# Performance work log

Hardware: AMD Instinct MI355X
Metric: run time of the kernel (lower is better)

Reference implementation:

```python
import jax, jax.numpy as jnp
import numpy as np

B, LQ, LP, H = 16, 2048, 2048, 1024

def setup_inputs() -> dict:
    key = jax.random.key(0)
    kq, kp, kw = jax.random.split(key, 3)
    q = jax.random.normal(kq, (B, LQ, H), dtype=jnp.float32)
    p = jax.random.normal(kp, (B, LP, H), dtype=jnp.float32)
    W = jax.random.normal(kw, (H, H), dtype=jnp.float32) * (1.0 / np.sqrt(H))
    b = jnp.zeros((H,), dtype=jnp.float32)
    return {"q": q, "p": p, "W": W, "b": b}

def reference(q, p, W, b):
    # shared linear + ReLU projections (torch Linear: x @ W.T + b)
    q_lin = jax.nn.relu(jnp.einsum('bqh,oh->bqo', q, W) + b)  # [B,LQ,H]
    p_lin = jax.nn.relu(jnp.einsum('bph,oh->bpo', p, W) + b)  # [B,LP,H]
    # unscaled cross-attention scores: p_lin @ q_lin^T -> [B,LP,LQ]
    scores = jnp.einsum('bpd,bqd->bpq', p_lin, q_lin)
    att = jax.nn.softmax(scores, axis=2)
    # context-aware query: att @ q_lin -> [B,LP,H]
    return jnp.einsum('bpq,bqd->bpd', att, q_lin)
```

## Files before the change

### kernel.cpp

```cpp
#include <hip/hip_runtime.h>


#define LQN 2048
#define LPN 2048
#define HD  1024
#define NBATCH 16

typedef _Float16 half8 __attribute__((ext_vector_type(8)));
typedef _Float16 half4_t __attribute__((ext_vector_type(4)));
typedef float f32x4 __attribute__((ext_vector_type(4)));

#define GLP(src, dst) __builtin_amdgcn_global_load_lds(                          \
    (const __attribute__((address_space(1))) void*)(src),                        \
    (__attribute__((address_space(3))) void*)(dst), 16, 0, 0)

__global__ __launch_bounds__(256) void cvt_f32_f16(const float* __restrict__ in,
                                                   _Float16* __restrict__ out,
                                                   long n4) {
  long i0 = (long)blockIdx.x * blockDim.x + threadIdx.x;
  long stride = (long)gridDim.x * blockDim.x;
  for (long i = i0; i < n4; i += stride) {
    float4 v = ((const float4*)in)[i];
    half4_t h = {(_Float16)v.x, (_Float16)v.y, (_Float16)v.z, (_Float16)v.w};
    ((half4_t*)out)[i] = h;
  }
}

__global__ __launch_bounds__(256) void transpose_k(const _Float16* __restrict__ in,
                                                   _Float16* __restrict__ out) {
  __shared__ _Float16 t[64][72];
  const int bz = blockIdx.z;
  const int q0 = blockIdx.x * 64;
  const int d0 = blockIdx.y * 64;
  const int tt = threadIdx.x;
  const int ql = tt & 63, dg = tt >> 6;
  const _Float16* src = in + ((size_t)bz * LQN + q0 + ql) * HD + d0 + dg * 16;
  half8 v0 = *(const half8*)(src);
  half8 v1 = *(const half8*)(src + 8);
  int g0 = (dg * 2) ^ (ql & 7);
  int g1 = (dg * 2 + 1) ^ (ql & 7);
  *(half8*)&t[ql][g0 * 8] = v0;
  *(half8*)&t[ql][g1 * 8] = v1;
  __syncthreads();
  const int dl = tt & 63, qg = tt >> 6;
  half8 o0, o1;
#pragma unroll
  for (int j = 0; j < 8; ++j) {
    int qq = qg * 16 + j;
    o0[j] = t[qq][(((dl >> 3) ^ (qq & 7)) << 3) + (dl & 7)];
  }
#pragma unroll
  for (int j = 0; j < 8; ++j) {
    int qq = qg * 16 + 8 + j;
    o1[j] = t[qq][(((dl >> 3) ^ (qq & 7)) << 3) + (dl & 7)];
  }
  _Float16* dst = out + ((size_t)bz * HD + d0 + dl) * LQN + q0 + qg * 16;
  *(half8*)dst = o0;
  *(half8*)(dst + 8) = o1;
}


#define SYNC_PRE                                        \
  __builtin_amdgcn_s_barrier();                         \
  __builtin_amdgcn_s_setprio(1);

#define SYNC_POST                                       \
  __builtin_amdgcn_s_setprio(0);                        \
  __builtin_amdgcn_s_barrier();                         \
  __builtin_amdgcn_sched_barrier(0);

#define SYNC_POST_VM                                    \
  __builtin_amdgcn_s_setprio(0);                        \
  asm volatile("s_waitcnt vmcnt(4)" ::: "memory");      \
  __builtin_amdgcn_s_barrier();                         \
  __builtin_amdgcn_sched_barrier(0);

#define LOADA(qm, buf)                                                            \
  _Pragma("unroll")                                                               \
  for (int mi = 0; mi < 4; ++mi) {                                                \
    areg[mi][0] = *(const half8*)(smA + (buf)*32768 + a0 + ((qm)*4+mi)*4096);     \
    areg[mi][1] = *(const half8*)(smA + (buf)*32768 + a1 + ((qm)*4+mi)*4096);     \
  }

#define LOADB(qn, buf)                                                            \
  _Pragma("unroll")                                                               \
  for (int ni = 0; ni < 2; ++ni) {                                                \
    bregs[qn][ni][0] = *(const half8*)(smB + (buf)*32768 + b0 + ((qn)*2+ni)*8192);\
    bregs[qn][ni][1] = *(const half8*)(smB + (buf)*32768 + b1 + ((qn)*2+ni)*8192);\
  }

#define STAGEA(t, h, buf) do {                                                    \
  GLP(gA + (size_t)((h)*128)*lda + (size_t)(t)*64,                                \
      smW + (buf)*32768 + (h)*16384 + wid*1024);                                  \
  GLP(gA + (size_t)((h)*128+64)*lda + (size_t)(t)*64,                             \
      smW + (buf)*32768 + (h)*16384 + 8192 + wid*1024);                           \
} while (0)

#define STAGEB(t, h, buf) do {                                                    \
  GLP(gB + (size_t)((h)*128)*ldb + (size_t)(t)*64,                                \
      smW + 65536 + (buf)*32768 + (h)*16384 + wid*1024);                          \
  GLP(gB + (size_t)((h)*128+64)*ldb + (size_t)(t)*64,                             \
      smW + 65536 + (buf)*32768 + (h)*16384 + 8192 + wid*1024);                   \
} while (0)

#define DO_MFMA(qm, qn)                                                           \
  _Pragma("unroll")                                                               \
  for (int mi = 0; mi < 4; ++mi) {                                                \
    _Pragma("unroll")                                                             \
    for (int ni = 0; ni < 2; ++ni) {                                              \
      acc[(qm)*4+mi][(qn)*2+ni] = __builtin_amdgcn_mfma_f32_16x16x32_f16(         \
          areg[mi][0], bregs[qn][ni][0], acc[(qm)*4+mi][(qn)*2+ni], 0, 0, 0);     \
      acc[(qm)*4+mi][(qn)*2+ni] = __builtin_amdgcn_mfma_f32_16x16x32_f16(         \
          areg[mi][1], bregs[qn][ni][1], acc[(qm)*4+mi][(qn)*2+ni], 0, 0, 0);     \
    }                                                                             \
  }

template <int EPI>
__global__ __launch_bounds__(512, 2) void gemm8p(
    const _Float16* __restrict__ A, const _Float16* __restrict__ B,
    const float* __restrict__ bias, void* __restrict__ Cv,
    float2* __restrict__ side, int K, int lda, int ldb, int ldc,
    long sAz, long sBz, long sCz) {
  extern __shared__ __align__(16) char smem[];
  const char* smA = smem;
  const char* smB = smem + 65536;
  char* smW = smem;

  const int tid = threadIdx.x;
  const int lane = tid & 63, wid = tid >> 6;
  const int l16 = lane & 15, lhi = lane >> 4;
  const int wr = wid >> 2, wcn = wid & 3;

  const int nx = gridDim.x;
  const int d = blockIdx.y * nx + blockIdx.x;
  const int cpx = (nx * gridDim.y) >> 3;
  const int t_ = (d & 7) * cpx + (d >> 3);
  const int xsh = 31 - __builtin_clz(nx);
  const int bn0 = (t_ & (nx - 1)) << 8;
  const int bm0 = (t_ >> xsh) << 8;

  const int mask = (l16 & 7) << 4;
  const int a0 = (wr * 2048 + l16 * 128 + lhi * 16) ^ mask;
  const int a1 = a0 ^ 64;
  const int b0 = (wcn * 2048 + l16 * 128 + lhi * 16) ^ mask;
  const int b1 = b0 ^ 64;

  const int srow = tid >> 3;
  const int scol = (((tid & 7) ^ ((tid >> 3) & 7)) << 3);

  const _Float16* gA = A + (size_t)blockIdx.z * sAz + (size_t)(bm0 + srow) * lda + scol;
  const _Float16* gB = B + (size_t)blockIdx.z * sBz + (size_t)(bn0 + srow) * ldb + scol;

  const int NT = K >> 6, NI = K >> 7;

  f32x4 acc[8][4] = {};
  half8 areg[4][2], bregs[2][2][2];

  STAGEA(0, 0, 0); STAGEB(0, 0, 0);
  STAGEA(0, 1, 0); STAGEB(0, 1, 0);
  STAGEA(1, 0, 1); STAGEB(1, 0, 1);
  __builtin_amdgcn_sched_barrier(0);
  asm volatile("s_waitcnt vmcnt(4)" ::: "memory");
  __builtin_amdgcn_s_barrier();
  __builtin_amdgcn_sched_barrier(0);

  for (int i = 0; i < NI; ++i) {
    const int t1 = 2 * i + 1;
    int t2 = 2 * i + 2; if (t2 > NT - 1) t2 = NT - 1;
    int t3 = 2 * i + 3; if (t3 > NT - 1) t3 = NT - 1;
    STAGEA(t1, 1, 1); LOADA(0, 0) LOADB(0, 0)
    SYNC_PRE DO_MFMA(0, 0) SYNC_POST
    STAGEB(t1, 1, 1); LOADB(1, 0)
    SYNC_PRE DO_MFMA(0, 1) SYNC_POST
    STAGEA(t2, 0, 0); LOADA(1, 0)
    SYNC_PRE DO_MFMA(1, 0) SYNC_POST
    STAGEB(t2, 0, 0);
    SYNC_PRE DO_MFMA(1, 1) SYNC_POST_VM
    STAGEA(t2, 1, 0); LOADA(0, 1) LOADB(0, 1)
    SYNC_PRE DO_MFMA(0, 0) SYNC_POST
    STAGEB(t2, 1, 0); LOADB(1, 1)
    SYNC_PRE DO_MFMA(0, 1) SYNC_POST
    STAGEA(t3, 0, 1); LOADA(1, 1)
    SYNC_PRE DO_MFMA(1, 0) SYNC_POST
    STAGEB(t3, 0, 1);
    SYNC_PRE DO_MFMA(1, 1) SYNC_POST_VM
  }

  if constexpr (EPI == 0) {
    float* Cb = (float*)Cv + (size_t)blockIdx.z * sCz;
#pragma unroll
    for (int m = 0; m < 8; ++m) {
      int row0 = bm0 + m * 32 + wr * 16 + lhi * 4;
#pragma unroll
      for (int n = 0; n < 4; ++n) {
        int col = bn0 + n * 64 + wcn * 16 + l16;
#pragma unroll
        for (int v = 0; v < 4; ++v)
          Cb[(size_t)(row0 + v) * ldc + col] = acc[m][n][v];
      }
    }
  } else if constexpr (EPI == 1) {
    _Float16* Cb = (_Float16*)Cv;
#pragma unroll
    for (int n = 0; n < 4; ++n) {
      int col = bn0 + n * 64 + wcn * 16 + l16;
      float bv = bias[col];
#pragma unroll
      for (int m = 0; m < 8; ++m) {
        int row0 = bm0 + m * 32 + wr * 16 + lhi * 4;
        Cb[(size_t)(row0 + 0) * ldc + col] = (_Float16)fmaxf(acc[m][n][0] + bv, 0.f);
        Cb[(size_t)(row0 + 1) * ldc + col] = (_Float16)fmaxf(acc[m][n][1] + bv, 0.f);
        Cb[(size_t)(row0 + 2) * ldc + col] = (_Float16)fmaxf(acc[m][n][2] + bv, 0.f);
        Cb[(size_t)(row0 + 3) * ldc + col] = (_Float16)fmaxf(acc[m][n][3] + bv, 0.f);
      }
    }
  } else {
    float* redm = (float*)smW;
    float* reds = (float*)(smW + 4096);
    float tm[8][4];
#pragma unroll
    for (int m = 0; m < 8; ++m)
#pragma unroll
      for (int v = 0; v < 4; ++v)
        tm[m][v] = fmaxf(fmaxf(acc[m][0][v], acc[m][1][v]),
                         fmaxf(acc[m][2][v], acc[m][3][v]));
#pragma unroll
    for (int o = 1; o < 16; o <<= 1)
#pragma unroll
      for (int m = 0; m < 8; ++m)
#pragma unroll
        for (int v = 0; v < 4; ++v)
          tm[m][v] = fmaxf(tm[m][v], __shfl_xor(tm[m][v], o));
    __syncthreads();
    if (l16 == 0) {
#pragma unroll
      for (int m = 0; m < 8; ++m)
#pragma unroll
        for (int v = 0; v < 4; ++v)
          redm[(m * 32 + wr * 16 + lhi * 4 + v) * 4 + wcn] = tm[m][v];
    }
    __syncthreads();
    float rm[8][4], rs[8][4];
#pragma unroll
    for (int m = 0; m < 8; ++m)
#pragma unroll
      for (int v = 0; v < 4; ++v) {
        float4 q4 = ((const float4*)redm)[m * 32 + wr * 16 + lhi * 4 + v];
        rm[m][v] = fmaxf(fmaxf(q4.x, q4.y), fmaxf(q4.z, q4.w));
      }
#pragma unroll
    for (int m = 0; m < 8; ++m)
#pragma unroll
      for (int v = 0; v < 4; ++v) {
        float s = 0.f;
#pragma unroll
        for (int n = 0; n < 4; ++n) {
          float e = __expf(acc[m][n][v] - rm[m][v]);
          acc[m][n][v] = e;
          s += e;
        }
        tm[m][v] = s;
      }
#pragma unroll
    for (int o = 1; o < 16; o <<= 1)
#pragma unroll
      for (int m = 0; m < 8; ++m)
#pragma unroll
        for (int v = 0; v < 4; ++v)
          tm[m][v] += __shfl_xor(tm[m][v], o);
    __syncthreads();
    if (l16 == 0) {
#pragma unroll
      for (int m = 0; m < 8; ++m)
#pragma unroll
        for (int v = 0; v < 4; ++v)
          reds[(m * 32 + wr * 16 + lhi * 4 + v) * 4 + wcn] = tm[m][v];
    }
    __syncthreads();
#pragma unroll
    for (int m = 0; m < 8; ++m)
#pragma unroll
      for (int v = 0; v < 4; ++v) {
        float4 q4 = ((const float4*)reds)[m * 32 + wr * 16 + lhi * 4 + v];
        rs[m][v] = (q4.x + q4.y) + (q4.z + q4.w);
      }
    _Float16* Cb = (_Float16*)Cv + (size_t)blockIdx.z * sCz;
#pragma unroll
    for (int n = 0; n < 4; ++n) {
      int col = bn0 + n * 64 + wcn * 16 + l16;
#pragma unroll
      for (int m = 0; m < 8; ++m) {
        int row0 = bm0 + m * 32 + wr * 16 + lhi * 4;
        Cb[(size_t)(row0 + 0) * ldc + col] = (_Float16)acc[m][n][0];
        Cb[(size_t)(row0 + 1) * ldc + col] = (_Float16)acc[m][n][1];
        Cb[(size_t)(row0 + 2) * ldc + col] = (_Float16)acc[m][n][2];
        Cb[(size_t)(row0 + 3) * ldc + col] = (_Float16)acc[m][n][3];
      }
    }
    if (l16 == 0 && wcn == 0) {
      float2* sb = side + ((size_t)blockIdx.z * 2048 + bm0) * 8 + (bn0 >> 8);
#pragma unroll
      for (int m = 0; m < 8; ++m)
#pragma unroll
        for (int v = 0; v < 4; ++v) {
          int r = m * 32 + wr * 16 + lhi * 4 + v;
          sb[(size_t)r * 8] = make_float2(rm[m][v], rs[m][v]);
        }
    }
  }
}

__global__ __launch_bounds__(256) void renorm_k(_Float16* __restrict__ P,
                                                const float2* __restrict__ side) {
  const int row = blockIdx.x;
  const int bz = blockIdx.y;
  const float2* sd = side + ((size_t)bz * 2048 + row) * 8;
  float mt[8], st[8];
#pragma unroll
  for (int t = 0; t < 8; ++t) { float2 v = sd[t]; mt[t] = v.x; st[t] = v.y; }
  float m = mt[0];
#pragma unroll
  for (int t = 1; t < 8; ++t) m = fmaxf(m, mt[t]);
  float S = 0.f;
#pragma unroll
  for (int t = 0; t < 8; ++t) S += st[t] * __expf(mt[t] - m);
  const float inv = 1.f / S;
  const int tid = threadIdx.x;
  const float sc = __expf(mt[tid >> 5] - m) * inv;
  _Float16* p = P + (((size_t)bz * 2048 + row) * 2048) + tid * 8;
  half8 v = *(half8*)p;
#pragma unroll
  for (int j = 0; j < 8; ++j) v[j] = (_Float16)((float)v[j] * sc);
  *(half8*)p = v;
}

extern "C" void kernel_launch(void* const* d_in, const int* in_sizes, int n_in,
                              void* d_out, int out_size, void* d_ws, size_t ws_size,
                              hipStream_t stream) {
  const float* q = (const float*)d_in[0];
  const float* p = (const float*)d_in[1];
  const float* W = (const float*)d_in[2];
  const float* bias = (const float*)d_in[3];
  float* out = (float*)d_out;
  char* ws = (char*)d_ws;

  _Float16* qf    = (_Float16*)(ws);
  _Float16* pf    = (_Float16*)(ws + 67108864L);
  _Float16* qlin  = (_Float16*)(ws + 134217728L);
  _Float16* plin  = (_Float16*)(ws + 201326592L);
  _Float16* qlinT = (_Float16*)(ws + 268435456L);
  _Float16* Wf    = (_Float16*)(ws + 335544320L);
  _Float16* Pbuf  = (_Float16*)(ws);
  float2*   side  = (float2*)(ws + 67108864L);

  const long nQ = (long)NBATCH * LQN * HD;
  const size_t SH = 131072;

  cvt_f32_f16<<<2048, 256, 0, stream>>>(q, qf, nQ / 4);
  cvt_f32_f16<<<2048, 256, 0, stream>>>(p, pf, nQ / 4);
  cvt_f32_f16<<<64, 256, 0, stream>>>(W, Wf, (long)HD * HD / 4);

  gemm8p<1><<<dim3(HD / 256, 2 * NBATCH * LQN / 256, 1), 512, SH, stream>>>(
      qf, Wf, bias, qlin, (float2*)0, HD, HD, HD, HD, 0, 0, 0);

  transpose_k<<<dim3(LQN / 64, HD / 64, NBATCH), 256, 0, stream>>>(qlin, qlinT);

  for (int c = 0; c < 2; ++c) {
    int bz0 = c * 8;
    gemm8p<2><<<dim3(LQN / 256, LPN / 256, 8), 512, SH, stream>>>(
        plin + (size_t)bz0 * LPN * HD, qlin + (size_t)bz0 * LQN * HD,
        (const float*)0, Pbuf, side,
        HD, HD, HD, LQN,
        (long)LPN * HD, (long)LQN * HD, (long)LPN * LQN);
    renorm_k<<<dim3(LPN, 8), 256, 0, stream>>>(Pbuf, side);
    gemm8p<0><<<dim3(HD / 256, LPN / 256, 8), 512, SH, stream>>>(
        Pbuf, qlinT + (size_t)bz0 * HD * LQN,
        (const float*)0, out + (size_t)bz0 * LPN * HD, (float2*)0,
        LQN, LQN, LQN, HD,
        (long)LPN * LQN, (long)HD * LQN, (long)LPN * HD);
  }
}
```

Measured before the change: 591.1 us.

## Fuse qlin transpose into projection epilogue and double-buffer GEMM fragment registers

The separate transpose kernel is removed. The projection GEMM epilogue now also writes qlin transposed as half4 stores for the q rows. The GEMM main loop is reorganised to use two sets of A/B register fragments, so LDS reads for the next sub-tile are issued one MFMA phase ahead of their use, with the staging order and vmcnt waits reshuffled to match. The aim is to save one kernel launch plus a full read and write of qlin, and to hide LDS latency behind MFMAs. The costs are higher register pressure and scattered strided transposed stores in the epilogue.

```diff
diff --git a/kernel.cpp b/kernel.cpp
--- a/kernel.cpp
+++ b/kernel.cpp
@@ -26,41 +26,9 @@
   }
 }
 
-__global__ __launch_bounds__(256) void transpose_k(const _Float16* __restrict__ in,
-                                                   _Float16* __restrict__ out) {
-  __shared__ _Float16 t[64][72];
-  const int bz = blockIdx.z;
-  const int q0 = blockIdx.x * 64;
-  const int d0 = blockIdx.y * 64;
-  const int tt = threadIdx.x;
-  const int ql = tt & 63, dg = tt >> 6;
-  const _Float16* src = in + ((size_t)bz * LQN + q0 + ql) * HD + d0 + dg * 16;
-  half8 v0 = *(const half8*)(src);
-  half8 v1 = *(const half8*)(src + 8);
-  int g0 = (dg * 2) ^ (ql & 7);
-  int g1 = (dg * 2 + 1) ^ (ql & 7);
-  *(half8*)&t[ql][g0 * 8] = v0;
-  *(half8*)&t[ql][g1 * 8] = v1;
-  __syncthreads();
-  const int dl = tt & 63, qg = tt >> 6;
-  half8 o0, o1;
-#pragma unroll
-  for (int j = 0; j < 8; ++j) {
-    int qq = qg * 16 + j;
-    o0[j] = t[qq][(((dl >> 3) ^ (qq & 7)) << 3) + (dl & 7)];
-  }
-#pragma unroll
-  for (int j = 0; j < 8; ++j) {
-    int qq = qg * 16 + 8 + j;
-    o1[j] = t[qq][(((dl >> 3) ^ (qq & 7)) << 3) + (dl & 7)];
-  }
-  _Float16* dst = out + ((size_t)bz * HD + d0 + dl) * LQN + q0 + qg * 16;
-  *(half8*)dst = o0;
-  *(half8*)(dst + 8) = o1;
-}
-
 
 #define SYNC_PRE                                        \
+  __builtin_amdgcn_sched_barrier(0);                    \
   __builtin_amdgcn_s_barrier();                         \
   __builtin_amdgcn_s_setprio(1);
 
@@ -75,18 +43,18 @@
   __builtin_amdgcn_s_barrier();                         \
   __builtin_amdgcn_sched_barrier(0);
 
-#define LOADA(qm, buf)                                                            \
+#define LOADA_TO(dst, qm, buf)                                                    \
   _Pragma("unroll")                                                               \
   for (int mi = 0; mi < 4; ++mi) {                                                \
-    areg[mi][0] = *(const half8*)(smA + (buf)*32768 + a0 + ((qm)*4+mi)*4096);     \
-    areg[mi][1] = *(const half8*)(smA + (buf)*32768 + a1 + ((qm)*4+mi)*4096);     \
-  }
-
-#define LOADB(qn, buf)                                                            \
+    dst[mi][0] = *(const half8*)(smA + (buf)*32768 + a0 + ((qm)*4+mi)*4096);      \
+    dst[mi][1] = *(const half8*)(smA + (buf)*32768 + a1 + ((qm)*4+mi)*4096);      \
+  }
+
+#define LOADB_TO(dst, qn, buf)                                                    \
   _Pragma("unroll")                                                               \
   for (int ni = 0; ni < 2; ++ni) {                                                \
-    bregs[qn][ni][0] = *(const half8*)(smB + (buf)*32768 + b0 + ((qn)*2+ni)*8192);\
-    bregs[qn][ni][1] = *(const half8*)(smB + (buf)*32768 + b1 + ((qn)*2+ni)*8192);\
+    dst[ni][0] = *(const half8*)(smB + (buf)*32768 + b0 + ((qn)*2+ni)*8192);      \
+    dst[ni][1] = *(const half8*)(smB + (buf)*32768 + b1 + ((qn)*2+ni)*8192);      \
   }
 
 #define STAGEA(t, h, buf) do {                                                    \
@@ -103,15 +71,15 @@
       smW + 65536 + (buf)*32768 + (h)*16384 + 8192 + wid*1024);                   \
 } while (0)
 
-#define DO_MFMA(qm, qn)                                                           \
+#define DO_MFMA2(aset, bset, qm, qn)                                              \
   _Pragma("unroll")                                                               \
   for (int mi = 0; mi < 4; ++mi) {                                                \
     _Pragma("unroll")                                                             \
     for (int ni = 0; ni < 2; ++ni) {                                              \
       acc[(qm)*4+mi][(qn)*2+ni] = __builtin_amdgcn_mfma_f32_16x16x32_f16(         \
-          areg[mi][0], bregs[qn][ni][0], acc[(qm)*4+mi][(qn)*2+ni], 0, 0, 0);     \
+          aset[mi][0], bset[ni][0], acc[(qm)*4+mi][(qn)*2+ni], 0, 0, 0);          \
       acc[(qm)*4+mi][(qn)*2+ni] = __builtin_amdgcn_mfma_f32_16x16x32_f16(         \
-          areg[mi][1], bregs[qn][ni][1], acc[(qm)*4+mi][(qn)*2+ni], 0, 0, 0);     \
+          aset[mi][1], bset[ni][1], acc[(qm)*4+mi][(qn)*2+ni], 0, 0, 0);          \
     }                                                                             \
   }
 
@@ -119,8 +87,8 @@
 __global__ __launch_bounds__(512, 2) void gemm8p(
     const _Float16* __restrict__ A, const _Float16* __restrict__ B,
     const float* __restrict__ bias, void* __restrict__ Cv,
-    float2* __restrict__ side, int K, int lda, int ldb, int ldc,
-    long sAz, long sBz, long sCz) {
+    _Float16* __restrict__ CT, float2* __restrict__ side,
+    int K, int lda, int ldb, int ldc, long sAz, long sBz, long sCz) {
   extern __shared__ __align__(16) char smem[];
   const char* smA = smem;
   const char* smB = smem + 65536;
@@ -154,36 +122,35 @@
   const int NT = K >> 6, NI = K >> 7;
 
   f32x4 acc[8][4] = {};
-  half8 areg[4][2], bregs[2][2][2];
-
-  STAGEA(0, 0, 0); STAGEB(0, 0, 0);
-  STAGEA(0, 1, 0); STAGEB(0, 1, 0);
-  STAGEA(1, 0, 1); STAGEB(1, 0, 1);
+  half8 aA0[4][2], aA1[4][2], bs0[2][2], bs1[2][2];
+
+  STAGEA(0, 0, 0); STAGEA(0, 1, 0); STAGEB(0, 0, 0); STAGEB(0, 1, 0);
+  STAGEA(1, 0, 1); STAGEA(1, 1, 1); STAGEB(1, 0, 1);
   __builtin_amdgcn_sched_barrier(0);
-  asm volatile("s_waitcnt vmcnt(4)" ::: "memory");
+  asm volatile("s_waitcnt vmcnt(6)" ::: "memory");
   __builtin_amdgcn_s_barrier();
   __builtin_amdgcn_sched_barrier(0);
+  LOADA_TO(aA0, 0, 0) LOADB_TO(bs0, 0, 0)
 
   for (int i = 0; i < NI; ++i) {
-    const int t1 = 2 * i + 1;
-    int t2 = 2 * i + 2; if (t2 > NT - 1) t2 = NT - 1;
-    int t3 = 2 * i + 3; if (t3 > NT - 1) t3 = NT - 1;
-    STAGEA(t1, 1, 1); LOADA(0, 0) LOADB(0, 0)
-    SYNC_PRE DO_MFMA(0, 0) SYNC_POST
-    STAGEB(t1, 1, 1); LOADB(1, 0)
-    SYNC_PRE DO_MFMA(0, 1) SYNC_POST
-    STAGEA(t2, 0, 0); LOADA(1, 0)
-    SYNC_PRE DO_MFMA(1, 0) SYNC_POST
-    STAGEB(t2, 0, 0);
-    SYNC_PRE DO_MFMA(1, 1) SYNC_POST_VM
-    STAGEA(t2, 1, 0); LOADA(0, 1) LOADB(0, 1)
-    SYNC_PRE DO_MFMA(0, 0) SYNC_POST
-    STAGEB(t2, 1, 0); LOADB(1, 1)
-    SYNC_PRE DO_MFMA(0, 1) SYNC_POST
-    STAGEA(t3, 0, 1); LOADA(1, 1)
-    SYNC_PRE DO_MFMA(1, 0) SYNC_POST
-    STAGEB(t3, 0, 1);
-    SYNC_PRE DO_MFMA(1, 1) SYNC_POST_VM
+    int t2c = 2 * i + 2; if (t2c > NT - 1) t2c = NT - 1;
+    int t3c = 2 * i + 3; if (t3c > NT - 1) t3c = NT - 1;
+    STAGEB(2 * i + 1, 1, 1); LOADB_TO(bs1, 1, 0) LOADA_TO(aA1, 1, 0)
+    SYNC_PRE DO_MFMA2(aA0, bs0, 0, 0) SYNC_POST
+    STAGEA(t2c, 0, 0);
+    SYNC_PRE DO_MFMA2(aA0, bs1, 0, 1) SYNC_POST
+    STAGEA(t2c, 1, 0);
+    SYNC_PRE DO_MFMA2(aA1, bs0, 1, 0) SYNC_POST_VM
+    STAGEB(t2c, 0, 0); LOADA_TO(aA0, 0, 1) LOADB_TO(bs0, 0, 1)
+    SYNC_PRE DO_MFMA2(aA1, bs1, 1, 1) SYNC_POST
+    STAGEB(t2c, 1, 0); LOADB_TO(bs1, 1, 1) LOADA_TO(aA1, 1, 1)
+    SYNC_PRE DO_MFMA2(aA0, bs0, 0, 0) SYNC_POST
+    STAGEA(t3c, 0, 1);
+    SYNC_PRE DO_MFMA2(aA0, bs1, 0, 1) SYNC_POST
+    STAGEA(t3c, 1, 1);
+    SYNC_PRE DO_MFMA2(aA1, bs0, 1, 0) SYNC_POST_VM
+    STAGEB(t3c, 0, 1); LOADA_TO(aA0, 0, 0) LOADB_TO(bs0, 0, 0)
+    SYNC_PRE DO_MFMA2(aA1, bs1, 1, 1) SYNC_POST
   }
 
   if constexpr (EPI == 0) {
@@ -201,6 +168,7 @@
     }
   } else if constexpr (EPI == 1) {
     _Float16* Cb = (_Float16*)Cv;
+    const bool doCT = (bm0 < NBATCH * LQN);
 #pragma unroll
     for (int n = 0; n < 4; ++n) {
       int col = bn0 + n * 64 + wcn * 16 + l16;
@@ -208,10 +176,19 @@
 #pragma unroll
       for (int m = 0; m < 8; ++m) {
         int row0 = bm0 + m * 32 + wr * 16 + lhi * 4;
-        Cb[(size_t)(row0 + 0) * ldc + col] = (_Float16)fmaxf(acc[m][n][0] + bv, 0.f);
-        Cb[(size_t)(row0 + 1) * ldc + col] = (_Float16)fmaxf(acc[m][n][1] + bv, 0.f);
-        Cb[(size_t)(row0 + 2) * ldc + col] = (_Float16)fmaxf(acc[m][n][2] + bv, 0.f);
-        Cb[(size_t)(row0 + 3) * ldc + col] = (_Float16)fmaxf(acc[m][n][3] + bv, 0.f);
+        float v0 = fmaxf(acc[m][n][0] + bv, 0.f);
+        float v1 = fmaxf(acc[m][n][1] + bv, 0.f);
+        float v2 = fmaxf(acc[m][n][2] + bv, 0.f);
+        float v3 = fmaxf(acc[m][n][3] + bv, 0.f);
+        Cb[(size_t)(row0 + 0) * ldc + col] = (_Float16)v0;
+        Cb[(size_t)(row0 + 1) * ldc + col] = (_Float16)v1;
+        Cb[(size_t)(row0 + 2) * ldc + col] = (_Float16)v2;
+        Cb[(size_t)(row0 + 3) * ldc + col] = (_Float16)v3;
+        if (doCT) {
+          half4_t h = {(_Float16)v0, (_Float16)v1, (_Float16)v2, (_Float16)v3};
+          int bz = row0 >> 11, qi = row0 & 2047;
+          *(half4_t*)&CT[(size_t)bz * ((size_t)HD * LQN) + (size_t)col * LQN + qi] = h;
+        }
       }
     }
   } else {
@@ -361,21 +338,19 @@
   cvt_f32_f16<<<64, 256, 0, stream>>>(W, Wf, (long)HD * HD / 4);
 
   gemm8p<1><<<dim3(HD / 256, 2 * NBATCH * LQN / 256, 1), 512, SH, stream>>>(
-      qf, Wf, bias, qlin, (float2*)0, HD, HD, HD, HD, 0, 0, 0);
-
-  transpose_k<<<dim3(LQN / 64, HD / 64, NBATCH), 256, 0, stream>>>(qlin, qlinT);
+      qf, Wf, bias, qlin, qlinT, (float2*)0, HD, HD, HD, HD, 0, 0, 0);
 
   for (int c = 0; c < 2; ++c) {
     int bz0 = c * 8;
     gemm8p<2><<<dim3(LQN / 256, LPN / 256, 8), 512, SH, stream>>>(
         plin + (size_t)bz0 * LPN * HD, qlin + (size_t)bz0 * LQN * HD,
-        (const float*)0, Pbuf, side,
+        (const float*)0, Pbuf, (_Float16*)0, side,
         HD, HD, HD, LQN,
         (long)LPN * HD, (long)LQN * HD, (long)LPN * LQN);
     renorm_k<<<dim3(LPN, 8), 256, 0, stream>>>(Pbuf, side);
     gemm8p<0><<<dim3(HD / 256, LPN / 256, 8), 512, SH, stream>>>(
         Pbuf, qlinT + (size_t)bz0 * HD * LQN,
-        (const float*)0, out + (size_t)bz0 * LPN * HD, (float2*)0,
+        (const float*)0, out + (size_t)bz0 * LPN * HD, (_Float16*)0, (float2*)0,
         LQN, LQN, LQN, HD,
         (long)LPN * LQN, (long)HD * LQN, (long)LPN * HD);
   }
```

Result: slower. 825.5 us (+39.7%).

## Merge GEMM pipeline phases to halve barriers per K-iteration

Applied to the files above, without the earlier changes.

Restructures the main GEMM loop from eight barrier-separated phases into four. Each phase now issues both A and B global-to-LDS stages, loads both B fragment sets, and runs two MFMA quadrants back to back. The aim is to cut the number of workgroup barriers and priority switches per iteration. In exchange, global-load issue and MFMA are interleaved less finely, and the vmcnt(4) wait now covers a different mix of loads.

```diff
diff --git a/kernel.cpp b/kernel.cpp
--- a/kernel.cpp
+++ b/kernel.cpp
@@ -75,18 +75,18 @@
   __builtin_amdgcn_s_barrier();                         \
   __builtin_amdgcn_sched_barrier(0);
 
-#define LOADA(qm, buf)                                                            \
+#define LOADA_TO(dst, qm, buf)                                                    \
   _Pragma("unroll")                                                               \
   for (int mi = 0; mi < 4; ++mi) {                                                \
-    areg[mi][0] = *(const half8*)(smA + (buf)*32768 + a0 + ((qm)*4+mi)*4096);     \
-    areg[mi][1] = *(const half8*)(smA + (buf)*32768 + a1 + ((qm)*4+mi)*4096);     \
-  }
-
-#define LOADB(qn, buf)                                                            \
+    dst[mi][0] = *(const half8*)(smA + (buf)*32768 + a0 + ((qm)*4+mi)*4096);      \
+    dst[mi][1] = *(const half8*)(smA + (buf)*32768 + a1 + ((qm)*4+mi)*4096);      \
+  }
+
+#define LOADB_TO(dst, qn, buf)                                                    \
   _Pragma("unroll")                                                               \
   for (int ni = 0; ni < 2; ++ni) {                                                \
-    bregs[qn][ni][0] = *(const half8*)(smB + (buf)*32768 + b0 + ((qn)*2+ni)*8192);\
-    bregs[qn][ni][1] = *(const half8*)(smB + (buf)*32768 + b1 + ((qn)*2+ni)*8192);\
+    dst[ni][0] = *(const half8*)(smB + (buf)*32768 + b0 + ((qn)*2+ni)*8192);      \
+    dst[ni][1] = *(const half8*)(smB + (buf)*32768 + b1 + ((qn)*2+ni)*8192);      \
   }
 
 #define STAGEA(t, h, buf) do {                                                    \
@@ -103,15 +103,15 @@
       smW + 65536 + (buf)*32768 + (h)*16384 + 8192 + wid*1024);                   \
 } while (0)
 
-#define DO_MFMA(qm, qn)                                                           \
+#define DO_MFMA2(aset, bset, qm, qn)                                              \
   _Pragma("unroll")                                                               \
   for (int mi = 0; mi < 4; ++mi) {                                                \
     _Pragma("unroll")                                                             \
     for (int ni = 0; ni < 2; ++ni) {                                              \
       acc[(qm)*4+mi][(qn)*2+ni] = __builtin_amdgcn_mfma_f32_16x16x32_f16(         \
-          areg[mi][0], bregs[qn][ni][0], acc[(qm)*4+mi][(qn)*2+ni], 0, 0, 0);     \
+          aset[mi][0], bset[ni][0], acc[(qm)*4+mi][(qn)*2+ni], 0, 0, 0);          \
       acc[(qm)*4+mi][(qn)*2+ni] = __builtin_amdgcn_mfma_f32_16x16x32_f16(         \
-          areg[mi][1], bregs[qn][ni][1], acc[(qm)*4+mi][(qn)*2+ni], 0, 0, 0);     \
+          aset[mi][1], bset[ni][1], acc[(qm)*4+mi][(qn)*2+ni], 0, 0, 0);          \
     }                                                                             \
   }
 
@@ -154,10 +154,9 @@
   const int NT = K >> 6, NI = K >> 7;
 
   f32x4 acc[8][4] = {};
-  half8 areg[4][2], bregs[2][2][2];
-
-  STAGEA(0, 0, 0); STAGEB(0, 0, 0);
-  STAGEA(0, 1, 0); STAGEB(0, 1, 0);
+  half8 aA[4][2], bs0[2][2], bs1[2][2];
+
+  STAGEA(0, 0, 0); STAGEA(0, 1, 0); STAGEB(0, 0, 0); STAGEB(0, 1, 0);
   STAGEA(1, 0, 1); STAGEB(1, 0, 1);
   __builtin_amdgcn_sched_barrier(0);
   asm volatile("s_waitcnt vmcnt(4)" ::: "memory");
@@ -166,24 +165,20 @@
 
   for (int i = 0; i < NI; ++i) {
     const int t1 = 2 * i + 1;
-    int t2 = 2 * i + 2; if (t2 > NT - 1) t2 = NT - 1;
-    int t3 = 2 * i + 3; if (t3 > NT - 1) t3 = NT - 1;
-    STAGEA(t1, 1, 1); LOADA(0, 0) LOADB(0, 0)
-    SYNC_PRE DO_MFMA(0, 0) SYNC_POST
-    STAGEB(t1, 1, 1); LOADB(1, 0)
-    SYNC_PRE DO_MFMA(0, 1) SYNC_POST
-    STAGEA(t2, 0, 0); LOADA(1, 0)
-    SYNC_PRE DO_MFMA(1, 0) SYNC_POST
-    STAGEB(t2, 0, 0);
-    SYNC_PRE DO_MFMA(1, 1) SYNC_POST_VM
-    STAGEA(t2, 1, 0); LOADA(0, 1) LOADB(0, 1)
-    SYNC_PRE DO_MFMA(0, 0) SYNC_POST
-    STAGEB(t2, 1, 0); LOADB(1, 1)
-    SYNC_PRE DO_MFMA(0, 1) SYNC_POST
-    STAGEA(t3, 0, 1); LOADA(1, 1)
-    SYNC_PRE DO_MFMA(1, 0) SYNC_POST
-    STAGEB(t3, 0, 1);
-    SYNC_PRE DO_MFMA(1, 1) SYNC_POST_VM
+    int t2c = 2 * i + 2; if (t2c > NT - 1) t2c = NT - 1;
+    int t3c = 2 * i + 3; if (t3c > NT - 1) t3c = NT - 1;
+    STAGEA(t1, 1, 1); STAGEB(t1, 1, 1);
+    LOADA_TO(aA, 0, 0) LOADB_TO(bs0, 0, 0) LOADB_TO(bs1, 1, 0)
+    SYNC_PRE DO_MFMA2(aA, bs0, 0, 0) DO_MFMA2(aA, bs1, 0, 1) SYNC_POST
+    STAGEA(t2c, 0, 0); STAGEB(t2c, 0, 0);
+    LOADA_TO(aA, 1, 0)
+    SYNC_PRE DO_MFMA2(aA, bs0, 1, 0) DO_MFMA2(aA, bs1, 1, 1) SYNC_POST_VM
+    STAGEA(t2c, 1, 0); STAGEB(t2c, 1, 0);
+    LOADA_TO(aA, 0, 1) LOADB_TO(bs0, 0, 1) LOADB_TO(bs1, 1, 1)
+    SYNC_PRE DO_MFMA2(aA, bs0, 0, 0) DO_MFMA2(aA, bs1, 0, 1) SYNC_POST
+    STAGEA(t3c, 0, 1); STAGEB(t3c, 0, 1);
+    LOADA_TO(aA, 1, 1)
+    SYNC_PRE DO_MFMA2(aA, bs0, 1, 0) DO_MFMA2(aA, bs1, 1, 1) SYNC_POST_VM
   }
 
   if constexpr (EPI == 0) {
```

Measured after the change: 593.1 us. About the same (+0.3%).

## Fuse fp32-to-fp16 input conversion into the shared linear projection GEMM

Applied to the files above, without the earlier changes.

Removes the separate conversion kernels for q and p. A new linear GEMM loads fp32 activations into registers, converts them to fp16 and writes them to LDS, with the A side software-pipelined across two LDS buffers, while W still streams in through global_load_lds. This avoids writing and rereading 128 MB of intermediate fp16 copies. In exchange the A loads pass through registers, which raises register pressure and adds VALU conversion work inside the main loop.

```diff
diff --git a/kernel.cpp b/kernel.cpp
--- a/kernel.cpp
+++ b/kernel.cpp
@@ -57,6 +57,151 @@
   _Float16* dst = out + ((size_t)bz * HD + d0 + dl) * LQN + q0 + qg * 16;
   *(half8*)dst = o0;
   *(half8*)(dst + 8) = o1;
+}
+
+
+#define LIN_LD(sg, tc) do {                                                       \
+  st[0] = *(const float4*)(gA32 + (size_t)((sg)*64) * 1024 + (size_t)(tc)*64);    \
+  st[1] = *(const float4*)(gA32 + (size_t)((sg)*64) * 1024 + (size_t)(tc)*64 + 4);\
+  st[2] = *(const float4*)(gA32 + (size_t)((sg)*64+64) * 1024 + (size_t)(tc)*64); \
+  st[3] = *(const float4*)(gA32 + (size_t)((sg)*64+64) * 1024 + (size_t)(tc)*64 + 4);\
+} while (0)
+
+#define LIN_WR(sg, buf) do {                                                      \
+  half8 h0, h1;                                                                   \
+  h0[0]=(_Float16)st[0].x; h0[1]=(_Float16)st[0].y;                               \
+  h0[2]=(_Float16)st[0].z; h0[3]=(_Float16)st[0].w;                               \
+  h0[4]=(_Float16)st[1].x; h0[5]=(_Float16)st[1].y;                               \
+  h0[6]=(_Float16)st[1].z; h0[7]=(_Float16)st[1].w;                               \
+  h1[0]=(_Float16)st[2].x; h1[1]=(_Float16)st[2].y;                               \
+  h1[2]=(_Float16)st[2].z; h1[3]=(_Float16)st[2].w;                               \
+  h1[4]=(_Float16)st[3].x; h1[5]=(_Float16)st[3].y;                               \
+  h1[6]=(_Float16)st[3].z; h1[7]=(_Float16)st[3].w;                               \
+  *(half8*)(smWr + (buf)*32768 + (sg)*8192 + tid*16) = h0;                        \
+  *(half8*)(smWr + (buf)*32768 + ((sg)+1)*8192 + tid*16) = h1;                    \
+} while (0)
+
+#define LIN_STB(tc, buf) do {                                                     \
+  GLP(gB + (size_t)(tc)*64,                      smWr + 65536 + (buf)*32768 + wid*1024);         \
+  GLP(gB + (size_t)64*1024  + (size_t)(tc)*64,   smWr + 65536 + (buf)*32768 +  8192 + wid*1024); \
+  GLP(gB + (size_t)128*1024 + (size_t)(tc)*64,   smWr + 65536 + (buf)*32768 + 16384 + wid*1024); \
+  GLP(gB + (size_t)192*1024 + (size_t)(tc)*64,   smWr + 65536 + (buf)*32768 + 24576 + wid*1024); \
+} while (0)
+
+#define LIN_LDA(qm, buf)                                                          \
+  _Pragma("unroll")                                                               \
+  for (int mi = 0; mi < 4; ++mi) {                                                \
+    aA[mi][0] = *(const half8*)(smA + (buf)*32768 + a0 + ((qm)*4+mi)*4096);       \
+    aA[mi][1] = *(const half8*)(smA + (buf)*32768 + a1 + ((qm)*4+mi)*4096);       \
+  }
+
+#define LIN_LDB(buf)                                                              \
+  _Pragma("unroll")                                                               \
+  for (int nb = 0; nb < 4; ++nb) {                                                \
+    bf[nb][0] = *(const half8*)(smB + (buf)*32768 + b0 + (nb)*8192);              \
+    bf[nb][1] = *(const half8*)(smB + (buf)*32768 + b1 + (nb)*8192);              \
+  }
+
+#define LIN_MFMA(qm)                                                              \
+  _Pragma("unroll")                                                               \
+  for (int mi = 0; mi < 4; ++mi) {                                                \
+    _Pragma("unroll")                                                             \
+    for (int nb = 0; nb < 4; ++nb) {                                              \
+      acc[(qm)*4+mi][nb] = __builtin_amdgcn_mfma_f32_16x16x32_f16(                \
+          aA[mi][0], bf[nb][0], acc[(qm)*4+mi][nb], 0, 0, 0);                     \
+      acc[(qm)*4+mi][nb] = __builtin_amdgcn_mfma_f32_16x16x32_f16(                \
+          aA[mi][1], bf[nb][1], acc[(qm)*4+mi][nb], 0, 0, 0);                     \
+    }                                                                             \
+  }
+
+__global__ __launch_bounds__(512, 2) void lin_gemm(
+    const float* __restrict__ Aq, const float* __restrict__ Ap,
+    const _Float16* __restrict__ Bw, const float* __restrict__ bias,
+    _Float16* __restrict__ C) {
+  extern __shared__ __align__(16) char smem[];
+  char* smWr = smem;
+  const char* smA = smem;
+  const char* smB = smem + 65536;
+
+  const int tid = threadIdx.x;
+  const int lane = tid & 63, wid = tid >> 6;
+  const int l16 = lane & 15, lhi = lane >> 4;
+  const int wr = wid >> 2, wcn = wid & 3;
+
+  const int nx = gridDim.x;
+  const int d = blockIdx.y * nx + blockIdx.x;
+  const int cpx = (nx * gridDim.y) >> 3;
+  const int t_ = (d & 7) * cpx + (d >> 3);
+  const int xsh = 31 - __builtin_clz(nx);
+  const int bn0 = (t_ & (nx - 1)) << 8;
+  const int bm0 = (t_ >> xsh) << 8;
+
+  const int mask = (l16 & 7) << 4;
+  const int a0 = (wr * 2048 + l16 * 128 + lhi * 16) ^ mask;
+  const int a1 = a0 ^ 64;
+  const int b0 = (wcn * 2048 + l16 * 128 + lhi * 16) ^ mask;
+  const int b1 = b0 ^ 64;
+
+  const int srow = tid >> 3;
+  const int scol = (((tid & 7) ^ ((tid >> 3) & 7)) << 3);
+
+  const float* gA32 = (bm0 < 32768 ? Aq + (size_t)(bm0 + srow) * 1024
+                                   : Ap + (size_t)(bm0 - 32768 + srow) * 1024) + scol;
+  const _Float16* gB = Bw + (size_t)(bn0 + srow) * 1024 + scol;
+
+  f32x4 acc[8][4] = {};
+  half8 aA[4][2], bf[4][2];
+  float4 st[4];
+
+  LIN_LD(0, 0);
+  asm volatile("s_waitcnt vmcnt(0)" ::: "memory");
+  LIN_WR(0, 0);
+  LIN_LD(2, 0);
+  LIN_STB(0, 0);
+  __builtin_amdgcn_sched_barrier(0);
+  asm volatile("s_waitcnt vmcnt(4)" ::: "memory");
+  LIN_WR(2, 0);
+  __syncthreads();
+
+  for (int t = 0; t < 16; ++t) {
+    const int cur = t & 1, nxt = cur ^ 1;
+    const int tc = (t < 15) ? t + 1 : 15;
+    LIN_LD(0, tc);
+    LIN_STB(tc, nxt);
+    __builtin_amdgcn_sched_barrier(0);
+    LIN_LDB(cur)
+    LIN_LDA(0, cur)
+    __builtin_amdgcn_s_setprio(1);
+    LIN_MFMA(0)
+    __builtin_amdgcn_s_setprio(0);
+    __builtin_amdgcn_sched_barrier(0);
+    asm volatile("s_waitcnt vmcnt(4)" ::: "memory");
+    LIN_WR(0, nxt);
+    LIN_LD(2, tc);
+    __builtin_amdgcn_sched_barrier(0);
+    LIN_LDA(1, cur)
+    __builtin_amdgcn_s_setprio(1);
+    LIN_MFMA(1)
+    __builtin_amdgcn_s_setprio(0);
+    __builtin_amdgcn_sched_barrier(0);
+    asm volatile("s_waitcnt vmcnt(0)" ::: "memory");
+    LIN_WR(2, nxt);
+    __syncthreads();
+  }
+
+#pragma unroll
+  for (int n = 0; n < 4; ++n) {
+    int col = bn0 + n * 64 + wcn * 16 + l16;
+    float bv = bias[col];
+#pragma unroll
+    for (int m = 0; m < 8; ++m) {
+      int row0 = bm0 + m * 32 + wr * 16 + lhi * 4;
+      C[(size_t)(row0 + 0) * 1024 + col] = (_Float16)fmaxf(acc[m][n][0] + bv, 0.f);
+      C[(size_t)(row0 + 1) * 1024 + col] = (_Float16)fmaxf(acc[m][n][1] + bv, 0.f);
+      C[(size_t)(row0 + 2) * 1024 + col] = (_Float16)fmaxf(acc[m][n][2] + bv, 0.f);
+      C[(size_t)(row0 + 3) * 1024 + col] = (_Float16)fmaxf(acc[m][n][3] + bv, 0.f);
+    }
+  }
 }
 
 
@@ -199,21 +344,6 @@
           Cb[(size_t)(row0 + v) * ldc + col] = acc[m][n][v];
       }
     }
-  } else if constexpr (EPI == 1) {
-    _Float16* Cb = (_Float16*)Cv;
-#pragma unroll
-    for (int n = 0; n < 4; ++n) {
-      int col = bn0 + n * 64 + wcn * 16 + l16;
-      float bv = bias[col];
-#pragma unroll
-      for (int m = 0; m < 8; ++m) {
-        int row0 = bm0 + m * 32 + wr * 16 + lhi * 4;
-        Cb[(size_t)(row0 + 0) * ldc + col] = (_Float16)fmaxf(acc[m][n][0] + bv, 0.f);
-        Cb[(size_t)(row0 + 1) * ldc + col] = (_Float16)fmaxf(acc[m][n][1] + bv, 0.f);
-        Cb[(size_t)(row0 + 2) * ldc + col] = (_Float16)fmaxf(acc[m][n][2] + bv, 0.f);
-        Cb[(size_t)(row0 + 3) * ldc + col] = (_Float16)fmaxf(acc[m][n][3] + bv, 0.f);
-      }
-    }
   } else {
     float* redm = (float*)smW;
     float* reds = (float*)(smW + 4096);
@@ -344,8 +474,6 @@
   float* out = (float*)d_out;
   char* ws = (char*)d_ws;
 
-  _Float16* qf    = (_Float16*)(ws);
-  _Float16* pf    = (_Float16*)(ws + 67108864L);
   _Float16* qlin  = (_Float16*)(ws + 134217728L);
   _Float16* plin  = (_Float16*)(ws + 201326592L);
   _Float16* qlinT = (_Float16*)(ws + 268435456L);
@@ -353,15 +481,12 @@
   _Float16* Pbuf  = (_Float16*)(ws);
   float2*   side  = (float2*)(ws + 67108864L);
 
-  const long nQ = (long)NBATCH * LQN * HD;
   const size_t SH = 131072;
 
-  cvt_f32_f16<<<2048, 256, 0, stream>>>(q, qf, nQ / 4);
-  cvt_f32_f16<<<2048, 256, 0, stream>>>(p, pf, nQ / 4);
   cvt_f32_f16<<<64, 256, 0, stream>>>(W, Wf, (long)HD * HD / 4);
 
-  gemm8p<1><<<dim3(HD / 256, 2 * NBATCH * LQN / 256, 1), 512, SH, stream>>>(
-      qf, Wf, bias, qlin, (float2*)0, HD, HD, HD, HD, 0, 0, 0);
+  lin_gemm<<<dim3(HD / 256, 2 * NBATCH * LQN / 256), 512, SH, stream>>>(
+      q, p, Wf, bias, qlin);
 
   transpose_k<<<dim3(LQN / 64, HD / 64, NBATCH), 256, 0, stream>>>(qlin, qlinT);
 
```

Result: no change. 590.4 us (-0.1%).
